# Kernel tuning notes

Hardware: AMD Instinct MI355X
Metric: run time of the kernel (lower is better)

## Reference

```python
import jax, jax.numpy as jnp
import numpy as np

N_NODES = 100000
N_EDGES = 1600000
NUM_FEATURES = 32
EDGE_DIM = 8
GAT_DIM = 16
HEADS = 4
HID = GAT_DIM * HEADS  # 64
OUT_DIM = 2
NUM_GRAPHS = 64
NEG_SLOPE = 0.2


def setup_inputs() -> dict:
    key = jax.random.key(0)
    ks = jax.random.split(key, 24)
    g = lambda k, shp, fan: jax.random.normal(k, shp, jnp.float32) * (1.0 / np.sqrt(fan))
    inp = {
        'x': jax.random.normal(ks[0], (N_NODES, NUM_FEATURES), jnp.float32),
        'edge_index': jax.random.randint(ks[1], (2, N_EDGES), 0, N_NODES, jnp.int64),
        'edge_attr': jax.random.normal(ks[2], (N_EDGES, EDGE_DIM), jnp.float32),
        'batch': jnp.sort(jax.random.randint(ks[3], (N_NODES,), 0, NUM_GRAPHS, jnp.int64)),
        # input GATConv params (PyG: lin bias-free, att_* of shape [H,C], bias [H*C])
        'W0': g(ks[4], (NUM_FEATURES, HID), NUM_FEATURES),
        'att_src0': g(ks[5], (HEADS, GAT_DIM), GAT_DIM),
        'att_dst0': g(ks[6], (HEADS, GAT_DIM), GAT_DIM),
        'We0': g(ks[7], (EDGE_DIM, HID), EDGE_DIM),
        'att_e0': g(ks[8], (HEADS, GAT_DIM), GAT_DIM),
        'b0': jnp.zeros((HID,), jnp.float32),
        # 2 hidden GATConv layers, stacked on a leading layer axis
        'Wh': g(ks[9], (2, HID, HID), HID),
        'att_src_h': g(ks[10], (2, HEADS, GAT_DIM), GAT_DIM),
        'att_dst_h': g(ks[11], (2, HEADS, GAT_DIM), GAT_DIM),
        'We_h': g(ks[12], (2, EDGE_DIM, HID), EDGE_DIM),
        'att_e_h': g(ks[13], (2, HEADS, GAT_DIM), GAT_DIM),
        'bh': jnp.zeros((2, HID), jnp.float32),
        # MLP head
        'fc1_w': g(ks[14], (HID, 2 * GAT_DIM), HID),
        'fc1_b': jnp.zeros((2 * GAT_DIM,), jnp.float32),
        'fc2_w': g(ks[15], (2 * GAT_DIM, OUT_DIM), 2 * GAT_DIM),
        'fc2_b': jnp.zeros((OUT_DIM,), jnp.float32),
    }
    return inp


def _gat_conv(x, src, dst, ea, W, a_s, a_d, We, a_e, b, n_nodes):
    # x: [N, Fin] -> out: [N, H*C]
    xp = (x @ W).reshape(n_nodes, HEADS, GAT_DIM)
    al_s = jnp.einsum('nhc,hc->nh', xp, a_s)            # per-node src logits
    al_d = jnp.einsum('nhc,hc->nh', xp, a_d)
    ep = (ea @ We).reshape(-1, HEADS, GAT_DIM)
    al_e = jnp.einsum('ehc,hc->eh', ep, a_e)
    alpha = jax.nn.leaky_relu(al_s[src] + al_d[dst] + al_e, NEG_SLOPE)  # [E,H]
    m = jax.ops.segment_max(alpha, dst, num_segments=n_nodes)
    m = jnp.where(jnp.isfinite(m), m, 0.0)              # nodes with no in-edges
    ex = jnp.exp(alpha - m[dst])
    den = jax.ops.segment_sum(ex, dst, num_segments=n_nodes)
    coef = ex / (den[dst] + 1e-16)                      # segment softmax over dst
    out = jax.ops.segment_sum(xp[src] * coef[..., None], dst, num_segments=n_nodes)
    return out.reshape(n_nodes, HID) + b


def _forward(x, edge_index, edge_attr, batch, W0, att_src0, att_dst0, We0, att_e0,
             b0, Wh, att_src_h, att_dst_h, We_h, att_e_h, bh, fc1_w, fc1_b, fc2_w, fc2_b):
    n = x.shape[0]
    src, dst = edge_index[0], edge_index[1]
    # PyG add_self_loops(fill_value='mean'): self-loop attr = mean of incoming edge attrs
    cnt = jax.ops.segment_sum(jnp.ones((src.shape[0],), x.dtype), dst, num_segments=n)
    mean_attr = jax.ops.segment_sum(edge_attr, dst, num_segments=n) / jnp.clip(cnt, 1.0)[:, None]
    loop = jnp.arange(n, dtype=src.dtype)
    src_sl = jnp.concatenate([src, loop])
    dst_sl = jnp.concatenate([dst, loop])
    ea_sl = jnp.concatenate([edge_attr, mean_attr], axis=0)

    h = _gat_conv(x, src_sl, dst_sl, ea_sl, W0, att_src0, att_dst0, We0, att_e0, b0, n)
    h = jax.nn.relu(h)
    for i in range(2):  # source has `x - F.relu(x)` (no-op): no ReLU between hidden layers
        h = _gat_conv(h, src_sl, dst_sl, ea_sl, Wh[i], att_src_h[i], att_dst_h[i],
                      We_h[i], att_e_h[i], bh[i], n)
    # global_mean_pool over graphs
    ones = jnp.ones((n,), h.dtype)
    gcnt = jax.ops.segment_sum(ones, batch, num_segments=NUM_GRAPHS)
    pooled = jax.ops.segment_sum(h, batch, num_segments=NUM_GRAPHS) / jnp.clip(gcnt, 1.0)[:, None]
    y = jax.nn.relu(pooled @ fc1_w + fc1_b)
    return y @ fc2_w + fc2_b


def reference(x, edge_index, edge_attr, batch, W0, att_src0, att_dst0, We0, att_e0,
              b0, Wh, att_src_h, att_dst_h, We_h, att_e_h, bh, fc1_w, fc1_b, fc2_w, fc2_b):
    return _forward(x, edge_index, edge_attr, batch, W0, att_src0, att_dst0, We0, att_e0,
                    b0, Wh, att_src_h, att_dst_h, We_h, att_e_h, bh, fc1_w, fc1_b, fc2_w, fc2_b)
```

## Files before the change

### kernel.cpp

```cpp
#include <hip/hip_runtime.h>
#include <hip/hip_bf16.h>
#include <hip/hip_fp16.h>

#define N_NODES 100000
#define N_EDGES 1600000
#define E_SL (N_EDGES + N_NODES)
#define HID 64
#define NUM_GRAPHS 64
#define NEG_SLOPE 0.2f
#define SCAN_CHUNK 1024
#define SCAN_NB ((N_NODES + SCAN_CHUNK - 1) / SCAN_CHUNK)
#define ROW_W 8
#define XP_NODES_PER_BLK 16
#define POOL_NODES_PER_BLK 256


__global__ void hist_kernel(const int* __restrict__ ei, int* __restrict__ cnt,
                            int* __restrict__ rank) {
    int e = blockIdx.x * blockDim.x + threadIdx.x;
    if (e >= N_EDGES) return;
    rank[e] = atomicAdd(&cnt[ei[N_EDGES + e]], 1);
}

__global__ void scan_local_kernel(const int* __restrict__ cnt, int* __restrict__ row_ptr,
                                  int* __restrict__ bsum) {
    __shared__ int s[256];
    int t = threadIdx.x;
    int base = blockIdx.x * SCAN_CHUNK + t * 4;
    int v[4]; int sum = 0;
    #pragma unroll
    for (int i = 0; i < 4; ++i) {
        int idx = base + i;
        v[i] = (idx < N_NODES) ? cnt[idx] + 1 : 0;
        sum += v[i];
    }
    s[t] = sum;
    __syncthreads();
    for (int off = 1; off < 256; off <<= 1) {
        int x = (t >= off) ? s[t - off] : 0;
        __syncthreads();
        s[t] += x;
        __syncthreads();
    }
    int run = s[t] - sum;
    #pragma unroll
    for (int i = 0; i < 4; ++i) {
        int idx = base + i;
        if (idx < N_NODES) row_ptr[idx] = run;
        run += v[i];
    }
    if (t == 255) bsum[blockIdx.x] = s[255];
}

__global__ void scan_bsum_kernel(int* __restrict__ bsum) {
    if (threadIdx.x != 0) return;
    int acc = 0;
    for (int i = 0; i < SCAN_NB; ++i) { int v = bsum[i]; bsum[i] = acc; acc += v; }
}

__global__ void scan_add_kernel(int* __restrict__ row_ptr, const int* __restrict__ bsum) {
    int i = blockIdx.x * blockDim.x + threadIdx.x;
    if (i > N_NODES) return;
    if (i == N_NODES) row_ptr[i] = E_SL;
    else row_ptr[i] += bsum[i >> 10];
}

__global__ void weff_all_kernel(const float* __restrict__ We0, const float* __restrict__ ae0,
                                const float* __restrict__ Weh, const float* __restrict__ aeh,
                                float* __restrict__ weff) {
    int t = threadIdx.x;
    if (t >= 96) return;
    int layer = t >> 5, r = t & 31;
    int dd = r >> 2, h = r & 3;
    const float* We = (layer == 0) ? We0 : Weh + (size_t)(layer - 1) * 8 * 64;
    const float* ae = (layer == 0) ? ae0 : aeh + (size_t)(layer - 1) * 64;
    float s = 0.f;
    #pragma unroll
    for (int c = 0; c < 16; ++c) s += We[dd * 64 + h * 16 + c] * ae[h * 16 + c];
    weff[layer * 32 + dd * 4 + h] = s;
}

__global__ void build_csr_kernel(const int* __restrict__ ei, const float* __restrict__ ea,
                                 const int* __restrict__ row_ptr,
                                 const int* __restrict__ rank,
                                 const float* __restrict__ weff,
                                 unsigned int* __restrict__ ale_csr) {
    int e = blockIdx.x * blockDim.x + threadIdx.x;
    if (e >= N_EDGES) return;
    int src = ei[e];
    int d = ei[N_EDGES + e];
    float4 a0 = *(const float4*)(ea + (size_t)e * 8);
    float4 a1 = *(const float4*)(ea + (size_t)e * 8 + 4);
    float av[8] = {a0.x, a0.y, a0.z, a0.w, a1.x, a1.y, a1.z, a1.w};
    unsigned int w[8];
    #pragma unroll
    for (int l = 0; l < 3; ++l) {
        float al[4];
        #pragma unroll
        for (int h = 0; h < 4; ++h) {
            float s = 0.f;
            #pragma unroll
            for (int j = 0; j < 8; ++j) s += av[j] * weff[l * 32 + j * 4 + h];
            al[h] = s;
        }
        __half2 p01 = __floats2half2_rn(al[0], al[1]);
        __half2 p23 = __floats2half2_rn(al[2], al[3]);
        w[2 * l]     = *(unsigned int*)&p01;
        w[2 * l + 1] = *(unsigned int*)&p23;
    }
    w[6] = (unsigned int)src;
    w[7] = 0u;
    int pos = row_ptr[d] + rank[e];
    unsigned int* rowp = ale_csr + (size_t)pos * ROW_W;
    *(uint4*)rowp       = make_uint4(w[0], w[1], w[2], w[3]);
    *(uint4*)(rowp + 4) = make_uint4(w[4], w[5], w[6], w[7]);
}

__global__ void mean_ea_kernel(const int* __restrict__ row_ptr,
                               unsigned int* __restrict__ ale_csr) {
    int idx = blockIdx.x * blockDim.x + threadIdx.x;
    if (idx >= N_NODES * 2) return;
    int n = idx >> 1, part = idx & 1;
    int start = row_ptr[n], last = row_ptr[n + 1] - 1;
    float inv = 1.f / fmaxf((float)(last - start), 1.f);
    if (part == 0) {
        float s[8] = {0.f, 0.f, 0.f, 0.f, 0.f, 0.f, 0.f, 0.f};
        for (int pos = start; pos < last; ++pos) {
            uint4 v = *(const uint4*)(ale_csr + (size_t)pos * ROW_W);
            float2 f0 = __half22float2(*(const __half2*)&v.x);
            float2 f1 = __half22float2(*(const __half2*)&v.y);
            float2 f2 = __half22float2(*(const __half2*)&v.z);
            float2 f3 = __half22float2(*(const __half2*)&v.w);
            s[0] += f0.x; s[1] += f0.y; s[2] += f1.x; s[3] += f1.y;
            s[4] += f2.x; s[5] += f2.y; s[6] += f3.x; s[7] += f3.y;
        }
        __half2 p0 = __floats2half2_rn(s[0] * inv, s[1] * inv);
        __half2 p1 = __floats2half2_rn(s[2] * inv, s[3] * inv);
        __half2 p2 = __floats2half2_rn(s[4] * inv, s[5] * inv);
        __half2 p3 = __floats2half2_rn(s[6] * inv, s[7] * inv);
        *(uint4*)(ale_csr + (size_t)last * ROW_W) =
            make_uint4(*(unsigned int*)&p0, *(unsigned int*)&p1,
                       *(unsigned int*)&p2, *(unsigned int*)&p3);
    } else {
        float s[4] = {0.f, 0.f, 0.f, 0.f};
        for (int pos = start; pos < last; ++pos) {
            uint2 v = *(const uint2*)(ale_csr + (size_t)pos * ROW_W + 4);
            float2 f0 = __half22float2(*(const __half2*)&v.x);
            float2 f1 = __half22float2(*(const __half2*)&v.y);
            s[0] += f0.x; s[1] += f0.y; s[2] += f1.x; s[3] += f1.y;
        }
        __half2 p0 = __floats2half2_rn(s[0] * inv, s[1] * inv);
        __half2 p1 = __floats2half2_rn(s[2] * inv, s[3] * inv);
        uint4 w = make_uint4(*(unsigned int*)&p0, *(unsigned int*)&p1,
                             (unsigned int)n, 0u);
        *(uint4*)(ale_csr + (size_t)last * ROW_W + 4) = w;
    }
}


template <int FIN>
__global__ __launch_bounds__(64) void xp_kernel(
    const float* __restrict__ xin, const float* __restrict__ W,
    const float* __restrict__ a_s, const float* __restrict__ a_d,
    __half* __restrict__ xp, float* __restrict__ als, float* __restrict__ ald) {
    int lane = threadIdx.x;
    float wcol[FIN];
    #pragma unroll
    for (int k = 0; k < FIN; ++k) wcol[k] = W[k * 64 + lane];
    float asl = a_s[lane], adl = a_d[lane];
    int n0 = blockIdx.x * XP_NODES_PER_BLK;
    #pragma unroll 1
    for (int ni = 0; ni < XP_NODES_PER_BLK; ++ni) {
        int n = n0 + ni;
        if (n >= N_NODES) return;
        const float* xr = xin + (size_t)n * FIN;
        float a0 = 0.f, a1 = 0.f, a2 = 0.f, a3 = 0.f;
        #pragma unroll
        for (int k = 0; k < FIN; k += 4) {
            float4 xv = *(const float4*)(xr + k);
            a0 += xv.x * wcol[k];     a1 += xv.y * wcol[k + 1];
            a2 += xv.z * wcol[k + 2]; a3 += xv.w * wcol[k + 3];
        }
        float acc = (a0 + a1) + (a2 + a3);
        xp[(size_t)n * 64 + lane] = __float2half(acc);
        float ps = acc * asl, pd = acc * adl;
        #pragma unroll
        for (int mk = 8; mk >= 1; mk >>= 1) {
            ps += __shfl_xor(ps, mk, 16);
            pd += __shfl_xor(pd, mk, 16);
        }
        if ((lane & 15) == 0) {
            als[(size_t)n * 4 + (lane >> 4)] = ps;
            ald[(size_t)n * 4 + (lane >> 4)] = pd;
        }
    }
}

__global__ __launch_bounds__(256) void gat_node_kernel(
    const int* __restrict__ row_ptr, const unsigned int* __restrict__ ale_csr,
    const float* __restrict__ als, const float* __restrict__ ald,
    const __half* __restrict__ xp, int layer,
    float* __restrict__ out, const float* __restrict__ bias, int relu_flag) {
    __shared__ float exl[4 * 256];
    __shared__ int   coll[4 * 64];
    int wave = threadIdx.x >> 6, lane = threadIdx.x & 63;
    int node = blockIdx.x * 4 + wave;
    if (node >= N_NODES) return;
    int start = row_ptr[node], end = row_ptr[node + 1];
    int deg = end - start;
    int wb = wave * 64, wb4 = wave * 256;
    int cq = lane & 15;
    int eg = lane >> 4;
    int hv = cq >> 2;

    float4 ad4 = *(const float4*)(ald + (size_t)node * 4);

    float4 acc4 = make_float4(0.f, 0.f, 0.f, 0.f);
    float csum = 0.f;

    for (int base = 0; base < deg; base += 64) {
        int cnt = min(64, deg - base);
        float ex0 = 0.f, ex1 = 0.f, ex2 = 0.f, ex3 = 0.f;
        int s = 0;
        if (lane < cnt) {
            const unsigned int* row = ale_csr + (size_t)(start + base + lane) * ROW_W;
            uint2 alew = *(const uint2*)(row + 2 * layer);
            s = (int)row[6];
            float2 e01 = __half22float2(*(const __half2*)&alew.x);
            float2 e23 = __half22float2(*(const __half2*)&alew.y);
            float4 as4 = *(const float4*)(als + (size_t)s * 4);
            float v0 = as4.x + ad4.x + e01.x;
            float v1 = as4.y + ad4.y + e01.y;
            float v2 = as4.z + ad4.z + e23.x;
            float v3 = as4.w + ad4.w + e23.y;
            ex0 = expf((v0 >= 0.f) ? v0 : NEG_SLOPE * v0);
            ex1 = expf((v1 >= 0.f) ? v1 : NEG_SLOPE * v1);
            ex2 = expf((v2 >= 0.f) ? v2 : NEG_SLOPE * v2);
            ex3 = expf((v3 >= 0.f) ? v3 : NEG_SLOPE * v3);
        }
        *(float4*)(exl + wb4 + lane * 4) = make_float4(ex0, ex1, ex2, ex3);
        coll[wb + lane] = s;
        const float* exw = exl + wb4 + hv;
        int cntUp = (cnt + 15) & ~15;
        for (int j = eg; j < cntUp; j += 16) {
            int s0 = coll[wb + j],     s1 = coll[wb + j + 4];
            int s2 = coll[wb + j + 8], s3 = coll[wb + j + 12];
            float c0 = exw[(j) * 4],      c1 = exw[(j + 4) * 4];
            float c2 = exw[(j + 8) * 4],  c3 = exw[(j + 12) * 4];
            uint2 x0 = *(const uint2*)(xp + (size_t)s0 * 64 + cq * 4);
            uint2 x1 = *(const uint2*)(xp + (size_t)s1 * 64 + cq * 4);
            uint2 x2 = *(const uint2*)(xp + (size_t)s2 * 64 + cq * 4);
            uint2 x3 = *(const uint2*)(xp + (size_t)s3 * 64 + cq * 4);
            float2 f00 = __half22float2(*(const __half2*)&x0.x);
            float2 f01 = __half22float2(*(const __half2*)&x0.y);
            float2 f10 = __half22float2(*(const __half2*)&x1.x);
            float2 f11 = __half22float2(*(const __half2*)&x1.y);
            float2 f20 = __half22float2(*(const __half2*)&x2.x);
            float2 f21 = __half22float2(*(const __half2*)&x2.y);
            float2 f30 = __half22float2(*(const __half2*)&x3.x);
            float2 f31 = __half22float2(*(const __half2*)&x3.y);
            acc4.x += c0 * f00.x + c1 * f10.x + c2 * f20.x + c3 * f30.x;
            acc4.y += c0 * f00.y + c1 * f10.y + c2 * f20.y + c3 * f30.y;
            acc4.z += c0 * f01.x + c1 * f11.x + c2 * f21.x + c3 * f31.x;
            acc4.w += c0 * f01.y + c1 * f11.y + c2 * f21.y + c3 * f31.y;
            csum   += c0 + c1 + c2 + c3;
        }
    }
    #pragma unroll
    for (int mk = 16; mk < 64; mk <<= 1) {
        acc4.x += __shfl_xor(acc4.x, mk);
        acc4.y += __shfl_xor(acc4.y, mk);
        acc4.z += __shfl_xor(acc4.z, mk);
        acc4.w += __shfl_xor(acc4.w, mk);
        csum   += __shfl_xor(csum, mk);
    }
    if (eg == 0) {
        float inv = 1.f / (csum + 1e-16f);
        float4 b4 = *(const float4*)(bias + cq * 4);
        float4 v;
        v.x = acc4.x * inv + b4.x;
        v.y = acc4.y * inv + b4.y;
        v.z = acc4.z * inv + b4.z;
        v.w = acc4.w * inv + b4.w;
        if (relu_flag) {
            v.x = fmaxf(v.x, 0.f); v.y = fmaxf(v.y, 0.f);
            v.z = fmaxf(v.z, 0.f); v.w = fmaxf(v.w, 0.f);
        }
        *(float4*)(out + (size_t)node * 64 + cq * 4) = v;
    }
}

__global__ void pool_kernel(const float* __restrict__ h, const int* __restrict__ batch,
                            float* __restrict__ pooled) {
    int base = blockIdx.x * POOL_NODES_PER_BLK;
    int tid = threadIdx.x;
    int c = tid & 63, r = tid >> 6;
    float acc = 0.f;
    int curg = -1;
    for (int i = r; i < POOL_NODES_PER_BLK; i += 4) {
        int n = base + i;
        if (n >= N_NODES) break;
        int g = batch[n];
        if (g != curg) {
            if (curg >= 0) atomicAdd(&pooled[curg * 64 + c], acc);
            curg = g; acc = 0.f;
        }
        acc += h[(size_t)n * 64 + c];
    }
    if (curg >= 0) atomicAdd(&pooled[curg * 64 + c], acc);
}

__global__ void mlp_kernel(const float* __restrict__ pooled, const int* __restrict__ batch,
                           const float* __restrict__ w1, const float* __restrict__ b1,
                           const float* __restrict__ w2, const float* __restrict__ b2,
                           float* __restrict__ y) {
    int g = blockIdx.x, t = threadIdx.x;
    __shared__ float p[64], f1[32];
    __shared__ float invc_s;
    if (t == 0) {
        int lo = 0, hi = N_NODES;
        while (lo < hi) { int mid = (lo + hi) >> 1; if (batch[mid] < g) lo = mid + 1; else hi = mid; }
        int start = lo;
        hi = N_NODES;
        while (lo < hi) { int mid = (lo + hi) >> 1; if (batch[mid] < g + 1) lo = mid + 1; else hi = mid; }
        invc_s = 1.f / fmaxf((float)(lo - start), 1.f);
    }
    __syncthreads();
    p[t] = pooled[g * 64 + t] * invc_s;
    __syncthreads();
    if (t < 32) {
        float a = b1[t];
        #pragma unroll
        for (int k = 0; k < 64; ++k) a += p[k] * w1[k * 32 + t];
        f1[t] = fmaxf(a, 0.f);
    }
    __syncthreads();
    if (t < 2) {
        float a = b2[t];
        #pragma unroll
        for (int k = 0; k < 32; ++k) a += f1[k] * w2[k * 2 + t];
        y[g * 2 + t] = a;
    }
}

extern "C" void kernel_launch(void* const* d_in, const int* in_sizes, int n_in,
                              void* d_out, int out_size, void* d_ws, size_t ws_size,
                              hipStream_t stream) {
    const float* x    = (const float*)d_in[0];
    const int*   ei   = (const int*)d_in[1];
    const float* ea   = (const float*)d_in[2];
    const int*   batch= (const int*)d_in[3];
    const float* W0   = (const float*)d_in[4];
    const float* as0  = (const float*)d_in[5];
    const float* ad0  = (const float*)d_in[6];
    const float* We0  = (const float*)d_in[7];
    const float* ae0  = (const float*)d_in[8];
    const float* b0   = (const float*)d_in[9];
    const float* Wh   = (const float*)d_in[10];
    const float* ash  = (const float*)d_in[11];
    const float* adh  = (const float*)d_in[12];
    const float* Weh  = (const float*)d_in[13];
    const float* aeh  = (const float*)d_in[14];
    const float* bh   = (const float*)d_in[15];
    const float* w1   = (const float*)d_in[16];
    const float* b1   = (const float*)d_in[17];
    const float* w2   = (const float*)d_in[18];
    const float* b2   = (const float*)d_in[19];
    float* out = (float*)d_out;

    char* wsb = (char*)d_ws;
    size_t off = 0;
    auto alloc = [&](size_t bytes) { char* p = wsb + off; off += (bytes + 255) & ~(size_t)255; return p; };
    int*          row_ptr = (int*)alloc((size_t)(N_NODES + 1) * 4);
    unsigned int* ale_csr = (unsigned int*)alloc((size_t)E_SL * ROW_W * 4);
    float*        als     = (float*)alloc((size_t)N_NODES * 4 * 4);
    float*        ald     = (float*)alloc((size_t)N_NODES * 4 * 4);
    float*        weff    = (float*)alloc(3 * 32 * 4);
    float*        pooled  = (float*)alloc((size_t)NUM_GRAPHS * 64 * 4);
    __half*       bufA    = (__half*)alloc((size_t)N_NODES * 64 * 2);
    float*        bufB    = (float*)alloc((size_t)N_NODES * 64 * 4);
    int* cnt  = (int*)bufB;
    int* bsum = cnt + N_NODES;
    int* rank = bsum + ((SCAN_NB + 63) & ~63);

    weff_all_kernel<<<1, 128, 0, stream>>>(We0, ae0, Weh, aeh, weff);
    hipMemsetAsync(cnt, 0, (size_t)N_NODES * 4, stream);
    hist_kernel<<<(N_EDGES + 255) / 256, 256, 0, stream>>>(ei, cnt, rank);
    scan_local_kernel<<<SCAN_NB, 256, 0, stream>>>(cnt, row_ptr, bsum);
    scan_bsum_kernel<<<1, 64, 0, stream>>>(bsum);
    scan_add_kernel<<<(N_NODES + 256) / 256, 256, 0, stream>>>(row_ptr, bsum);
    build_csr_kernel<<<(N_EDGES + 255) / 256, 256, 0, stream>>>(
        ei, ea, row_ptr, rank, weff, ale_csr);
    mean_ea_kernel<<<(N_NODES * 2 + 255) / 256, 256, 0, stream>>>(row_ptr, ale_csr);

    for (int layer = 0; layer < 3; ++layer) {
        const float *W, *as_, *ad_, *bb, *xin;
        int relu_flag = (layer == 0);
        if (layer == 0) {
            W = W0; as_ = as0; ad_ = ad0; bb = b0; xin = x;
        } else {
            int i = layer - 1;
            W   = Wh  + (size_t)i * 64 * 64;
            as_ = ash + (size_t)i * 64;
            ad_ = adh + (size_t)i * 64;
            bb  = bh  + (size_t)i * 64;
            xin = bufB;
        }
        int xpgrid = (N_NODES + XP_NODES_PER_BLK - 1) / XP_NODES_PER_BLK;
        if (layer == 0)
            xp_kernel<32><<<xpgrid, 64, 0, stream>>>(xin, W, as_, ad_, bufA, als, ald);
        else
            xp_kernel<64><<<xpgrid, 64, 0, stream>>>(xin, W, as_, ad_, bufA, als, ald);
        gat_node_kernel<<<(N_NODES + 3) / 4, 256, 0, stream>>>(
            row_ptr, ale_csr, als, ald, bufA, layer, bufB, bb, relu_flag);
    }
    hipMemsetAsync(pooled, 0, (size_t)NUM_GRAPHS * 64 * 4, stream);
    pool_kernel<<<(N_NODES + POOL_NODES_PER_BLK - 1) / POOL_NODES_PER_BLK, 256, 0, stream>>>(
        bufB, batch, pooled);
    mlp_kernel<<<NUM_GRAPHS, 64, 0, stream>>>(pooled, batch, w1, b1, w2, b2, out);
}
```

Baseline: 625.3 us.

## Fuse layer-0 projection into CSR build kernel and split edge rows across lane pairs

Merges the layer-0 node projection (xp, source and destination logits) into the CSR build launch, interleaving one projection block per two edge-build blocks so the two independent jobs share a single grid. The edge build now uses two threads per edge, each loading half the edge attributes, exchanging them by shuffle, and writing one 16-byte half of the CSR row. This removes a kernel launch and spreads per-edge work across more threads, at the cost of block-type divergence and extra shuffles. It relies on N_EDGES being divisible by 128.

After: 616.0 us. No clear change (-1.5%).

```diff
diff --git a/kernel.cpp b/kernel.cpp
--- a/kernel.cpp
+++ b/kernel.cpp
@@ -13,6 +13,8 @@
 #define ROW_W 8
 #define XP_NODES_PER_BLK 16
 #define POOL_NODES_PER_BLK 256
+#define BUILD_NB (N_EDGES / 128)
+#define XP0_NB ((N_NODES + 15) / 16)
 
 
 __global__ void hist_kernel(const int* __restrict__ ei, int* __restrict__ cnt,
@@ -80,40 +82,98 @@
     weff[layer * 32 + dd * 4 + h] = s;
 }
 
-__global__ void build_csr_kernel(const int* __restrict__ ei, const float* __restrict__ ea,
-                                 const int* __restrict__ row_ptr,
-                                 const int* __restrict__ rank,
-                                 const float* __restrict__ weff,
-                                 unsigned int* __restrict__ ale_csr) {
-    int e = blockIdx.x * blockDim.x + threadIdx.x;
-    if (e >= N_EDGES) return;
-    int src = ei[e];
+__global__ __launch_bounds__(256) void build_xp0_kernel(
+    const int* __restrict__ ei, const float* __restrict__ ea,
+    const int* __restrict__ row_ptr, const int* __restrict__ rank,
+    const float* __restrict__ weff, unsigned int* __restrict__ ale_csr,
+    const float* __restrict__ x, const float* __restrict__ W0,
+    const float* __restrict__ a_s, const float* __restrict__ a_d,
+    __half* __restrict__ xp, float* __restrict__ als, float* __restrict__ ald) {
+    int b = blockIdx.x;
+    int g = b / 3, r3 = b - g * 3;
+    if (r3 == 2) {
+        int wave = threadIdx.x >> 6, lane = threadIdx.x & 63;
+        float wcol[32];
+        #pragma unroll
+        for (int k = 0; k < 32; ++k) wcol[k] = W0[k * 64 + lane];
+        float asl = a_s[lane], adl = a_d[lane];
+        int n0 = g * XP_NODES_PER_BLK + wave * 4;
+        #pragma unroll 1
+        for (int ni = 0; ni < 4; ++ni) {
+            int n = n0 + ni;
+            if (n >= N_NODES) return;
+            const float* xr = x + (size_t)n * 32;
+            float a0 = 0.f, a1 = 0.f, a2 = 0.f, a3 = 0.f;
+            #pragma unroll
+            for (int k = 0; k < 32; k += 4) {
+                float4 xv = *(const float4*)(xr + k);
+                a0 += xv.x * wcol[k];     a1 += xv.y * wcol[k + 1];
+                a2 += xv.z * wcol[k + 2]; a3 += xv.w * wcol[k + 3];
+            }
+            float acc = (a0 + a1) + (a2 + a3);
+            xp[(size_t)n * 64 + lane] = __float2half(acc);
+            float ps = acc * asl, pd = acc * adl;
+            #pragma unroll
+            for (int mk = 8; mk >= 1; mk >>= 1) {
+                ps += __shfl_xor(ps, mk, 16);
+                pd += __shfl_xor(pd, mk, 16);
+            }
+            if ((lane & 15) == 0) {
+                als[(size_t)n * 4 + (lane >> 4)] = ps;
+                ald[(size_t)n * 4 + (lane >> 4)] = pd;
+            }
+        }
+        return;
+    }
+    int build_b = g * 2 + r3;
+    int e = build_b * 128 + (threadIdx.x >> 1);
+    int q = threadIdx.x & 1;
     int d = ei[N_EDGES + e];
-    float4 a0 = *(const float4*)(ea + (size_t)e * 8);
-    float4 a1 = *(const float4*)(ea + (size_t)e * 8 + 4);
-    float av[8] = {a0.x, a0.y, a0.z, a0.w, a1.x, a1.y, a1.z, a1.w};
-    unsigned int w[8];
-    #pragma unroll
-    for (int l = 0; l < 3; ++l) {
+    float4 a = *((const float4*)(ea + (size_t)e * 8) + q);
+    float o0 = __shfl_xor(a.x, 1), o1 = __shfl_xor(a.y, 1);
+    float o2 = __shfl_xor(a.z, 1), o3 = __shfl_xor(a.w, 1);
+    float av[8];
+    av[0] = q ? o0 : a.x;  av[1] = q ? o1 : a.y;
+    av[2] = q ? o2 : a.z;  av[3] = q ? o3 : a.w;
+    av[4] = q ? a.x : o0;  av[5] = q ? a.y : o1;
+    av[6] = q ? a.z : o2;  av[7] = q ? a.w : o3;
+    unsigned int w[4];
+    if (q == 0) {
+        float al[8];
+        #pragma unroll
+        for (int l = 0; l < 2; ++l) {
+            #pragma unroll
+            for (int h = 0; h < 4; ++h) {
+                float s = 0.f;
+                #pragma unroll
+                for (int j = 0; j < 8; ++j) s += av[j] * weff[l * 32 + j * 4 + h];
+                al[l * 4 + h] = s;
+            }
+        }
+        __half2 p0 = __floats2half2_rn(al[0], al[1]);
+        __half2 p1 = __floats2half2_rn(al[2], al[3]);
+        __half2 p2 = __floats2half2_rn(al[4], al[5]);
+        __half2 p3 = __floats2half2_rn(al[6], al[7]);
+        w[0] = *(unsigned int*)&p0; w[1] = *(unsigned int*)&p1;
+        w[2] = *(unsigned int*)&p2; w[3] = *(unsigned int*)&p3;
+    } else {
         float al[4];
         #pragma unroll
         for (int h = 0; h < 4; ++h) {
             float s = 0.f;
             #pragma unroll
-            for (int j = 0; j < 8; ++j) s += av[j] * weff[l * 32 + j * 4 + h];
+            for (int j = 0; j < 8; ++j) s += av[j] * weff[64 + j * 4 + h];
             al[h] = s;
         }
-        __half2 p01 = __floats2half2_rn(al[0], al[1]);
-        __half2 p23 = __floats2half2_rn(al[2], al[3]);
-        w[2 * l]     = *(unsigned int*)&p01;
-        w[2 * l + 1] = *(unsigned int*)&p23;
-    }
-    w[6] = (unsigned int)src;
-    w[7] = 0u;
+        __half2 p0 = __floats2half2_rn(al[0], al[1]);
+        __half2 p1 = __floats2half2_rn(al[2], al[3]);
+        w[0] = *(unsigned int*)&p0; w[1] = *(unsigned int*)&p1;
+        w[2] = (unsigned int)ei[e];
+        w[3] = 0u;
+    }
     int pos = row_ptr[d] + rank[e];
-    unsigned int* rowp = ale_csr + (size_t)pos * ROW_W;
-    *(uint4*)rowp       = make_uint4(w[0], w[1], w[2], w[3]);
-    *(uint4*)(rowp + 4) = make_uint4(w[4], w[5], w[6], w[7]);
+    *(uint4*)(ale_csr + (size_t)pos * ROW_W + q * 4) =
+        make_uint4(w[0], w[1], w[2], w[3]);
 }
 
 __global__ void mean_ea_kernel(const int* __restrict__ row_ptr,
@@ -389,28 +449,25 @@
     scan_local_kernel<<<SCAN_NB, 256, 0, stream>>>(cnt, row_ptr, bsum);
     scan_bsum_kernel<<<1, 64, 0, stream>>>(bsum);
     scan_add_kernel<<<(N_NODES + 256) / 256, 256, 0, stream>>>(row_ptr, bsum);
-    build_csr_kernel<<<(N_EDGES + 255) / 256, 256, 0, stream>>>(
-        ei, ea, row_ptr, rank, weff, ale_csr);
+    build_xp0_kernel<<<BUILD_NB + XP0_NB, 256, 0, stream>>>(
+        ei, ea, row_ptr, rank, weff, ale_csr,
+        x, W0, as0, ad0, bufA, als, ald);
     mean_ea_kernel<<<(N_NODES * 2 + 255) / 256, 256, 0, stream>>>(row_ptr, ale_csr);
 
     for (int layer = 0; layer < 3; ++layer) {
-        const float *W, *as_, *ad_, *bb, *xin;
+        const float *bb;
         int relu_flag = (layer == 0);
         if (layer == 0) {
-            W = W0; as_ = as0; ad_ = ad0; bb = b0; xin = x;
+            bb = b0;
         } else {
             int i = layer - 1;
-            W   = Wh  + (size_t)i * 64 * 64;
-            as_ = ash + (size_t)i * 64;
-            ad_ = adh + (size_t)i * 64;
+            const float* W   = Wh  + (size_t)i * 64 * 64;
+            const float* as_ = ash + (size_t)i * 64;
+            const float* ad_ = adh + (size_t)i * 64;
             bb  = bh  + (size_t)i * 64;
-            xin = bufB;
-        }
-        int xpgrid = (N_NODES + XP_NODES_PER_BLK - 1) / XP_NODES_PER_BLK;
-        if (layer == 0)
-            xp_kernel<32><<<xpgrid, 64, 0, stream>>>(xin, W, as_, ad_, bufA, als, ald);
-        else
-            xp_kernel<64><<<xpgrid, 64, 0, stream>>>(xin, W, as_, ad_, bufA, als, ald);
+            int xpgrid = (N_NODES + XP_NODES_PER_BLK - 1) / XP_NODES_PER_BLK;
+            xp_kernel<64><<<xpgrid, 64, 0, stream>>>(bufB, W, as_, ad_, bufA, als, ald);
+        }
         gat_node_kernel<<<(N_NODES + 3) / 4, 256, 0, stream>>>(
             row_ptr, ale_csr, als, ald, bufA, layer, bufB, bb, relu_flag);
     }
```
